# Performance work log

Measured on AMD Instinct MI355X. Metric: run time of the kernel, lower is better.

The kernel has to match this reference:

```python
import jax, jax.numpy as jnp
import numpy as np

N_NODES = 100000
N_EDGES = 1600000
G_DIM, H1, H2 = 128, 64, 32
HEADS = 4
NUM_REL = 3
NUM_CLASSES = 7


def setup_inputs() -> dict:
    key = jax.random.key(0)
    ks = jax.random.split(key, 16)
    s = 0.05
    inp = {
        "x": jax.random.normal(ks[0], (N_NODES, G_DIM), dtype=jnp.float32),
        "lengths": N_NODES,
        "edge_index": jax.random.randint(ks[1], (2, N_EDGES), 0, N_NODES),
        "edge_type": jax.random.randint(ks[2], (N_EDGES,), 0, NUM_REL),
        # RGCNConv params (root weight + per-relation weights + bias)
        "W_rel": jax.random.normal(ks[3], (NUM_REL, G_DIM, H1), dtype=jnp.float32) * s,
        "W_root": jax.random.normal(ks[4], (G_DIM, H1), dtype=jnp.float32) * s,
        "b_rgcn": jax.random.normal(ks[5], (H1,), dtype=jnp.float32) * s,
        # TransformerConv params (heads*H2 = 128 output, concat=True default)
        "Wq": jax.random.normal(ks[6], (H1, HEADS * H2), dtype=jnp.float32) * s,
        "bq": jax.random.normal(ks[7], (HEADS * H2,), dtype=jnp.float32) * s,
        "Wk": jax.random.normal(ks[8], (H1, HEADS * H2), dtype=jnp.float32) * s,
        "bk": jax.random.normal(ks[9], (HEADS * H2,), dtype=jnp.float32) * s,
        "Wv": jax.random.normal(ks[10], (H1, HEADS * H2), dtype=jnp.float32) * s,
        "bv": jax.random.normal(ks[11], (HEADS * H2,), dtype=jnp.float32) * s,
        "Wskip": jax.random.normal(ks[12], (H1, HEADS * H2), dtype=jnp.float32) * s,
        "bskip": jax.random.normal(ks[13], (HEADS * H2,), dtype=jnp.float32) * s,
        # final classifier (in = heads*H2 since TransformerConv concat=True)
        "Wf": jax.random.normal(ks[14], (HEADS * H2, NUM_CLASSES), dtype=jnp.float32) * s,
        "bf": jax.random.normal(ks[15], (NUM_CLASSES,), dtype=jnp.float32) * s,
    }
    return inp


def _forward(x, edge_index, edge_type, W_rel, W_root, b_rgcn,
             Wq, bq, Wk, bk, Wv, bv, Wskip, bskip, Wf, bf):
    n = x.shape[0]
    src, dst = edge_index[0], edge_index[1]  # source -> target flow

    # ---- RGCNConv: root transform + per-relation mean aggregation ----
    h = x @ W_root + b_rgcn  # [N, H1]
    for r in range(NUM_REL):
        hr = x @ W_rel[r]  # [N, H1] transform at node level (cheap)
        mask = (edge_type == r)
        msg = jnp.where(mask[:, None], hr[src], 0.0)  # [E, H1]
        ssum = jax.ops.segment_sum(msg, dst, num_segments=n)
        cnt = jax.ops.segment_sum(mask.astype(x.dtype), dst, num_segments=n)
        h = h + jnp.where(cnt[:, None] > 0, ssum / jnp.maximum(cnt, 1.0)[:, None], 0.0)
    h = jax.nn.relu(h)

    # ---- TransformerConv (heads=4, concat=True, root skip) ----
    Q = (h @ Wq + bq).reshape(n, HEADS, H2)
    K = (h @ Wk + bk).reshape(n, HEADS, H2)
    V = (h @ Wv + bv).reshape(n, HEADS, H2)
    scores = jnp.sum(Q[dst] * K[src], axis=-1) / jnp.sqrt(jnp.asarray(H2, x.dtype))  # [E, HEADS]
    smax = jax.ops.segment_max(scores, dst, num_segments=n)  # [N, HEADS]
    e = jnp.exp(scores - smax[dst])
    denom = jax.ops.segment_sum(e, dst, num_segments=n)  # [N, HEADS]
    alpha = e / jnp.maximum(denom[dst], 1e-16)  # [E, HEADS]
    agg = jax.ops.segment_sum(alpha[..., None] * V[src], dst, num_segments=n)  # [N, HEADS, H2]
    out = agg.reshape(n, HEADS * H2) + h @ Wskip + bskip
    out = jax.nn.relu(out)

    return out @ Wf + bf  # [N, NUM_CLASSES]


def reference(x, lengths, edge_index, edge_type, W_rel, W_root, b_rgcn,
              Wq, bq, Wk, bk, Wv, bv, Wskip, bskip, Wf, bf):
    # lengths is accepted but unused by the original forward
    return _forward(x, edge_index, edge_type, W_rel, W_root, b_rgcn,
                    Wq, bq, Wk, bk, Wv, bv, Wskip, bskip, Wf, bf)
```

## Files before the change

kernel.cpp:

```cpp
#include <hip/hip_runtime.h>
#include <math.h>

#define N_NODES 100000
#define N_EDGES 1600000

typedef short short8 __attribute__((ext_vector_type(8)));
typedef float f32x4 __attribute__((ext_vector_type(4)));

static __device__ __forceinline__ float bf2f(unsigned int u16) {
    return __uint_as_float(u16 << 16);
}
static __device__ __forceinline__ unsigned short f2bf(float f) {
    unsigned u = __float_as_uint(f);
    unsigned r = u + 0x7FFF + ((u >> 16) & 1);
    return (unsigned short)(r >> 16);
}
static __device__ __forceinline__ void unpack8(uint4 u, float* f) {
    f[0] = bf2f(u.x & 0xFFFF); f[1] = bf2f(u.x >> 16);
    f[2] = bf2f(u.y & 0xFFFF); f[3] = bf2f(u.y >> 16);
    f[4] = bf2f(u.z & 0xFFFF); f[5] = bf2f(u.z >> 16);
    f[6] = bf2f(u.w & 0xFFFF); f[7] = bf2f(u.w >> 16);
}
static __device__ __forceinline__ void unpack4(uint2 u, float* f) {
    f[0] = bf2f(u.x & 0xFFFF); f[1] = bf2f(u.x >> 16);
    f[2] = bf2f(u.y & 0xFFFF); f[3] = bf2f(u.y >> 16);
}

__global__ void repack_kernel(const float* __restrict__ Wrel, const float* __restrict__ Wroot,
                              const float* __restrict__ Wq, const float* __restrict__ Wk,
                              const float* __restrict__ Wv, const float* __restrict__ Wsk,
                              const float* __restrict__ bq, const float* __restrict__ bk,
                              const float* __restrict__ bv, const float* __restrict__ bsk,
                              unsigned short* __restrict__ W1t, unsigned short* __restrict__ W2t,
                              float* __restrict__ bcat) {
    int idx = blockIdx.x * 256 + threadIdx.x;
    if (idx < 128 * 256) {
        int k = idx >> 8, c = idx & 255;
        float v;
        if (c < 192) { int r = c >> 6, cc = c & 63; v = Wrel[r * 8192 + k * 64 + cc]; }
        else v = Wroot[k * 64 + (c - 192)];
        W1t[c * 128 + k] = f2bf(v);
    }
    int i2 = idx - 128 * 256;
    if (i2 >= 0 && i2 < 64 * 512) {
        int k = i2 >> 9, c = i2 & 511;
        float v;
        if (c < 128) v = Wq[k * 128 + c];
        else if (c < 256) v = Wk[k * 128 + c - 128];
        else if (c < 384) v = Wv[k * 128 + c - 256];
        else v = Wsk[k * 128 + c - 384];
        W2t[c * 64 + k] = f2bf(v);
    }
    int i3 = idx - 128 * 256 - 64 * 512;
    if (i3 >= 0 && i3 < 512) {
        float v;
        if (i3 < 128) v = bq[i3];
        else if (i3 < 256) v = bk[i3 - 128];
        else if (i3 < 384) v = bv[i3 - 256];
        else v = bsk[i3 - 384];
        bcat[i3] = v;
    }
}

__global__ void hist_kernel(const int* __restrict__ ei, const int* __restrict__ et,
                            int* __restrict__ cntr) {
    int e = blockIdx.x * 256 + threadIdx.x;
    if (e < N_EDGES) atomicAdd(&cntr[et[e] * N_NODES + ei[N_EDGES + e]], 1);
}

__global__ void scanA_kernel(const int* __restrict__ cntr, int* __restrict__ part) {
    __shared__ int wsum[4];
    int t = threadIdx.x;
    int base = blockIdx.x * 1024 + t * 4;
    int s = 0;
    for (int i = 0; i < 4; i++) {
        int idx = base + i;
        if (idx < N_NODES) s += cntr[idx] + cntr[N_NODES + idx] + cntr[2 * N_NODES + idx];
    }
    for (int off = 1; off < 64; off <<= 1) s += __shfl_xor(s, off);
    if ((t & 63) == 0) wsum[t >> 6] = s;
    __syncthreads();
    if (t == 0) part[blockIdx.x] = wsum[0] + wsum[1] + wsum[2] + wsum[3];
}

__global__ void scanC_kernel(const int* __restrict__ cntr, const int* __restrict__ part,
                             int* __restrict__ rs) {
    __shared__ int wsum[4];
    __shared__ int ws2[4];
    int t = threadIdx.x;
    int lane = t & 63;
    int base = blockIdx.x * 1024 + t * 4;
    int v[4]; int tsum = 0;
    for (int i = 0; i < 4; i++) {
        int idx = base + i;
        v[i] = (idx < N_NODES) ? (cntr[idx] + cntr[N_NODES + idx] + cntr[2 * N_NODES + idx]) : 0;
        tsum += v[i];
    }
    int p = (t < blockIdx.x) ? part[t] : 0;
    for (int off = 1; off < 64; off <<= 1) p += __shfl_xor(p, off);
    if (lane == 0) ws2[t >> 6] = p;
    int x = tsum;
    for (int off = 1; off < 64; off <<= 1) { int y = __shfl_up(x, off); if (lane >= off) x += y; }
    if (lane == 63) wsum[t >> 6] = x;
    __syncthreads();
    if (t == 0) { int run = 0; for (int w = 0; w < 4; w++) { int tmp = wsum[w]; wsum[w] = run; run += tmp; } }
    __syncthreads();
    int bofs = ws2[0] + ws2[1] + ws2[2] + ws2[3];
    int excl = x - tsum + wsum[t >> 6] + bofs;
    for (int i = 0; i < 4; i++) {
        int idx = base + i;
        if (idx < N_NODES) rs[idx] = excl;
        excl += v[i];
    }
    if (blockIdx.x == 0 && t == 0) rs[N_NODES] = N_EDGES;
}

__global__ void scatter_kernel(const int* __restrict__ ei, const int* __restrict__ et,
                               const int* __restrict__ rs, const int* __restrict__ cntr,
                               int* __restrict__ fill,
                               unsigned int* __restrict__ ep, float* __restrict__ epw) {
    int e = blockIdx.x * 256 + threadIdx.x;
    if (e >= N_EDGES) return;
    int src = ei[e], dst = ei[N_EDGES + e], r = et[e];
    int pos = rs[dst] + atomicAdd(&fill[dst], 1);
    int c = cntr[r * N_NODES + dst];
    ep[pos] = ((unsigned)src << 2) | (unsigned)r;
    epw[pos] = 1.f / (float)c;
}

__global__ __launch_bounds__(256) void gemm1_mfma(const float* __restrict__ X,
                                                  const unsigned short* __restrict__ W1t,
                                                  unsigned short* __restrict__ hr_all) {
    __shared__ unsigned short As[64][136];
    __shared__ unsigned short Bs[64][136];
    int t = threadIdx.x;
    int rb = blockIdx.x * 64;
    #pragma unroll
    for (int i = 0; i < 8; i++) {
        int lin = t + i * 256;
        int row = lin >> 5;
        int c4 = lin & 31;
        float4 v = make_float4(0.f, 0.f, 0.f, 0.f);
        int gr = rb + row;
        if (gr < N_NODES) v = *(const float4*)&X[gr * 128 + c4 * 4];
        unsigned w0 = (unsigned)f2bf(v.x) | ((unsigned)f2bf(v.y) << 16);
        unsigned w1 = (unsigned)f2bf(v.z) | ((unsigned)f2bf(v.w) << 16);
        *(uint2*)&As[row][c4 * 4] = make_uint2(w0, w1);
    }
    int w = t >> 6, l = t & 63;
    int wr = (w >> 1) * 32, wc = (w & 1) * 32;
    int lr = l & 15, lk = (l >> 4) * 8;
    int drow = (l >> 4) * 4;
    int dcol = l & 15;
    for (int cb4 = 0; cb4 < 4; cb4++) {
        int cb = cb4 * 64;
        __syncthreads();
        #pragma unroll
        for (int i = 0; i < 4; i++) {
            int lin = t + i * 256;
            int n = lin >> 4;
            int k8 = lin & 15;
            *(uint4*)&Bs[n][k8 * 8] = *(const uint4*)&W1t[(cb + n) * 128 + k8 * 8];
        }
        __syncthreads();
        f32x4 c00 = {0.f,0.f,0.f,0.f}, c01 = {0.f,0.f,0.f,0.f};
        f32x4 c10 = {0.f,0.f,0.f,0.f}, c11 = {0.f,0.f,0.f,0.f};
        #pragma unroll
        for (int kk = 0; kk < 128; kk += 32) {
            short8 a0 = *(const short8*)&As[wr + lr][kk + lk];
            short8 a1 = *(const short8*)&As[wr + 16 + lr][kk + lk];
            short8 b0 = *(const short8*)&Bs[wc + lr][kk + lk];
            short8 b1 = *(const short8*)&Bs[wc + 16 + lr][kk + lk];
            c00 = __builtin_amdgcn_mfma_f32_16x16x32_bf16(a0, b0, c00, 0, 0, 0);
            c01 = __builtin_amdgcn_mfma_f32_16x16x32_bf16(a0, b1, c01, 0, 0, 0);
            c10 = __builtin_amdgcn_mfma_f32_16x16x32_bf16(a1, b0, c10, 0, 0, 0);
            c11 = __builtin_amdgcn_mfma_f32_16x16x32_bf16(a1, b1, c11, 0, 0, 0);
        }
        f32x4 cc[2][2] = {{c00, c01}, {c10, c11}};
        #pragma unroll
        for (int i = 0; i < 2; i++)
            #pragma unroll
            for (int j = 0; j < 2; j++)
                #pragma unroll
                for (int rg = 0; rg < 4; rg++) {
                    int gr = rb + wr + i * 16 + drow + rg;
                    int gc = cb + wc + j * 16 + dcol;
                    if (gr < N_NODES) hr_all[gr * 256 + gc] = f2bf(cc[i][j][rg]);
                }
    }
}

__global__ __launch_bounds__(256) void rgcn_kernel(const unsigned short* __restrict__ hr,
                                                   const float* __restrict__ brg, const int* __restrict__ rs,
                                                   const unsigned int* __restrict__ ep,
                                                   const float* __restrict__ epw,
                                                   unsigned short* __restrict__ Hm) {
    int t = threadIdx.x, lane = t & 63;
    int n = blockIdx.x * 4 + (t >> 6);
    if (n >= N_NODES) return;
    int slot = lane >> 4, pos = lane & 15;
    const uint2* H2 = (const uint2*)hr;
    float a0 = 0.f, a1 = 0.f, a2 = 0.f, a3 = 0.f;
    int p0 = rs[n], p1 = rs[n + 1];
    for (int base = p0; base < p1; base += 64) {
        int pc = base + lane;
        unsigned chunk = (pc < p1) ? ep[pc] : 0u;
        float wch = (pc < p1) ? epw[pc] : 0.f;
        int cnt = min(64, p1 - base);
        for (int g0 = 0; g0 < cnt; g0 += 8) {
            int iA = g0 + slot, iB = iA + 4;
            unsigned eA = (unsigned)__shfl((int)chunk, iA);
            unsigned eB = (unsigned)__shfl((int)chunk, iB);
            float wA = __shfl(wch, iA);
            float wB = __shfl(wch, iB);
            uint2 hA = H2[eA * 16 + pos];
            uint2 hB = H2[eB * 16 + pos];
            float f[4];
            unpack4(hA, f);
            a0 += wA * f[0]; a1 += wA * f[1]; a2 += wA * f[2]; a3 += wA * f[3];
            unpack4(hB, f);
            a0 += wB * f[0]; a1 += wB * f[1]; a2 += wB * f[2]; a3 += wB * f[3];
        }
    }
    a0 += __shfl_xor(a0, 16); a0 += __shfl_xor(a0, 32);
    a1 += __shfl_xor(a1, 16); a1 += __shfl_xor(a1, 32);
    a2 += __shfl_xor(a2, 16); a2 += __shfl_xor(a2, 32);
    a3 += __shfl_xor(a3, 16); a3 += __shfl_xor(a3, 32);
    uint2 rt = H2[(n * 4 + 3) * 16 + pos];
    float rtf[4]; unpack4(rt, rtf);
    float4 bb = ((const float4*)brg)[pos];
    float h0 = fmaxf(rtf[0] + bb.x + a0, 0.f);
    float h1 = fmaxf(rtf[1] + bb.y + a1, 0.f);
    float h2 = fmaxf(rtf[2] + bb.z + a2, 0.f);
    float h3 = fmaxf(rtf[3] + bb.w + a3, 0.f);
    if (slot == 0) {
        uint2 wv;
        wv.x = (unsigned)f2bf(h0) | ((unsigned)f2bf(h1) << 16);
        wv.y = (unsigned)f2bf(h2) | ((unsigned)f2bf(h3) << 16);
        ((uint2*)Hm)[n * 16 + pos] = wv;
    }
}

__global__ __launch_bounds__(256) void gemm2_mfma(const unsigned short* __restrict__ Hm,
                                                  const unsigned short* __restrict__ W2t,
                                                  const float* __restrict__ bcat,
                                                  unsigned short* __restrict__ Qb, unsigned short* __restrict__ Kb,
                                                  unsigned short* __restrict__ Vb, unsigned short* __restrict__ Sb) {
    __shared__ unsigned short As[64][72];
    __shared__ unsigned short Bs[64][72];
    int t = threadIdx.x;
    int rb = blockIdx.x * 64;
    #pragma unroll
    for (int i = 0; i < 2; i++) {
        int lin = t + i * 256;
        int row = lin >> 3;
        int k8 = lin & 7;
        uint4 v = make_uint4(0, 0, 0, 0);
        int gr = rb + row;
        if (gr < N_NODES) v = *(const uint4*)&Hm[gr * 64 + k8 * 8];
        *(uint4*)&As[row][k8 * 8] = v;
    }
    int w = t >> 6, l = t & 63;
    int wr = (w >> 1) * 32, wc = (w & 1) * 32;
    int lr = l & 15, lk = (l >> 4) * 8;
    int drow = (l >> 4) * 4;
    int dcol = l & 15;
    for (int cb8 = 0; cb8 < 8; cb8++) {
        int cb = cb8 * 64;
        __syncthreads();
        #pragma unroll
        for (int i = 0; i < 2; i++) {
            int lin = t + i * 256;
            int n = lin >> 3;
            int k8 = lin & 7;
            *(uint4*)&Bs[n][k8 * 8] = *(const uint4*)&W2t[(cb + n) * 64 + k8 * 8];
        }
        __syncthreads();
        f32x4 c00 = {0.f,0.f,0.f,0.f}, c01 = {0.f,0.f,0.f,0.f};
        f32x4 c10 = {0.f,0.f,0.f,0.f}, c11 = {0.f,0.f,0.f,0.f};
        #pragma unroll
        for (int kk = 0; kk < 64; kk += 32) {
            short8 a0 = *(const short8*)&As[wr + lr][kk + lk];
            short8 a1 = *(const short8*)&As[wr + 16 + lr][kk + lk];
            short8 b0 = *(const short8*)&Bs[wc + lr][kk + lk];
            short8 b1 = *(const short8*)&Bs[wc + 16 + lr][kk + lk];
            c00 = __builtin_amdgcn_mfma_f32_16x16x32_bf16(a0, b0, c00, 0, 0, 0);
            c01 = __builtin_amdgcn_mfma_f32_16x16x32_bf16(a0, b1, c01, 0, 0, 0);
            c10 = __builtin_amdgcn_mfma_f32_16x16x32_bf16(a1, b0, c10, 0, 0, 0);
            c11 = __builtin_amdgcn_mfma_f32_16x16x32_bf16(a1, b1, c11, 0, 0, 0);
        }
        f32x4 cc[2][2] = {{c00, c01}, {c10, c11}};
        #pragma unroll
        for (int i = 0; i < 2; i++)
            #pragma unroll
            for (int j = 0; j < 2; j++)
                #pragma unroll
                for (int rg = 0; rg < 4; rg++) {
                    int gr = rb + wr + i * 16 + drow + rg;
                    int gc = cb + wc + j * 16 + dcol;
                    if (gr >= N_NODES) continue;
                    float v = cc[i][j][rg] + bcat[gc];
                    unsigned short h = f2bf(v);
                    if (gc < 128) Qb[gr * 128 + gc] = h;
                    else if (gc < 256) Kb[gr * 128 + (gc - 128)] = h;
                    else if (gc < 384) Vb[gr * 128 + (gc - 256)] = h;
                    else Sb[gr * 128 + (gc - 384)] = h;
                }
    }
}

__global__ __launch_bounds__(256) void attn_kernel(const unsigned short* __restrict__ Qb,
                                                   const unsigned short* __restrict__ Kb,
                                                   const unsigned short* __restrict__ Vb,
                                                   const int* __restrict__ rs, const unsigned int* __restrict__ ep,
                                                   const unsigned short* __restrict__ Sb,
                                                   const float* __restrict__ Wf, const float* __restrict__ bfv,
                                                   float* __restrict__ out) {
    int t = threadIdx.x, lane = t & 63;
    int n = blockIdx.x * 4 + (t >> 6);
    if (n >= N_NODES) return;
    int slot = lane >> 4, pos = lane & 15;
    const uint4* K4 = (const uint4*)Kb;
    const uint4* V4 = (const uint4*)Vb;
    const float qs = 0.17677669529663687f;
    uint4 qv = ((const uint4*)Qb)[n * 16 + pos];
    float q[8]; unpack8(qv, q);
    #pragma unroll
    for (int i = 0; i < 8; i++) q[i] *= qs;
    float o[8] = {0.f,0.f,0.f,0.f,0.f,0.f,0.f,0.f};
    float d = 0.f;
    int p0 = rs[n], p1 = rs[n + 1];
    for (int base = p0; base < p1; base += 64) {
        int pc = base + lane;
        unsigned chunk = (pc < p1) ? ep[pc] : 0u;
        int cnt = min(64, p1 - base);
        for (int g0 = 0; g0 < cnt; g0 += 8) {
            int iA = g0 + slot, iB = iA + 4;
            unsigned eA = (unsigned)__shfl((int)chunk, iA);
            unsigned eB = (unsigned)__shfl((int)chunk, iB);
            int sA = (int)(eA >> 2), sB = (int)(eB >> 2);
            uint4 kA = K4[sA * 16 + pos];
            uint4 vA = V4[sA * 16 + pos];
            uint4 kB = K4[sB * 16 + pos];
            uint4 vB = V4[sB * 16 + pos];
            float kf[8], vf[8];
            unpack8(kA, kf);
            float dotA = q[0]*kf[0] + q[1]*kf[1] + q[2]*kf[2] + q[3]*kf[3]
                       + q[4]*kf[4] + q[5]*kf[5] + q[6]*kf[6] + q[7]*kf[7];
            dotA += __shfl_xor(dotA, 1);
            dotA += __shfl_xor(dotA, 2);
            float wA = __expf(dotA);
            wA = (iA < cnt) ? wA : 0.f;
            unpack8(kB, kf);
            float dotB = q[0]*kf[0] + q[1]*kf[1] + q[2]*kf[2] + q[3]*kf[3]
                       + q[4]*kf[4] + q[5]*kf[5] + q[6]*kf[6] + q[7]*kf[7];
            dotB += __shfl_xor(dotB, 1);
            dotB += __shfl_xor(dotB, 2);
            float wB = __expf(dotB);
            wB = (iB < cnt) ? wB : 0.f;
            d += wA + wB;
            unpack8(vA, vf);
            #pragma unroll
            for (int i = 0; i < 8; i++) o[i] += wA * vf[i];
            unpack8(vB, vf);
            #pragma unroll
            for (int i = 0; i < 8; i++) o[i] += wB * vf[i];
        }
    }
    d += __shfl_xor(d, 16); d += __shfl_xor(d, 32);
    #pragma unroll
    for (int i = 0; i < 8; i++) { o[i] += __shfl_xor(o[i], 16); o[i] += __shfl_xor(o[i], 32); }
    float inv = (d > 0.f) ? 1.f / d : 0.f;
    uint4 sv = ((const uint4*)Sb)[n * 16 + pos];
    float sf[8]; unpack8(sv, sf);
    float rf[8];
    #pragma unroll
    for (int i = 0; i < 8; i++) rf[i] = fmaxf(sf[i] + o[i] * inv, 0.f);
    float rr0 = (slot == 0) ? rf[0] : (slot == 1) ? rf[2] : (slot == 2) ? rf[4] : rf[6];
    float rr1 = (slot == 0) ? rf[1] : (slot == 1) ? rf[3] : (slot == 2) ? rf[5] : rf[7];
    int gd = pos * 8 + slot * 2;
    float acc[7];
    #pragma unroll
    for (int j = 0; j < 7; j++) acc[j] = rr0 * Wf[gd * 7 + j] + rr1 * Wf[gd * 7 + 7 + j];
    #pragma unroll
    for (int j = 0; j < 7; j++) {
        acc[j] += __shfl_xor(acc[j], 1);
        acc[j] += __shfl_xor(acc[j], 2);
        acc[j] += __shfl_xor(acc[j], 4);
        acc[j] += __shfl_xor(acc[j], 8);
        acc[j] += __shfl_xor(acc[j], 16);
        acc[j] += __shfl_xor(acc[j], 32);
    }
    if (lane == 0) {
        #pragma unroll
        for (int j = 0; j < 7; j++) out[n * 7 + j] = acc[j] + bfv[j];
    }
}

extern "C" void kernel_launch(void* const* d_in, const int* in_sizes, int n_in,
                              void* d_out, int out_size, void* d_ws, size_t ws_size,
                              hipStream_t stream) {
    const float* x     = (const float*)d_in[0];
    const int*   ei    = (const int*)d_in[2];
    const int*   et    = (const int*)d_in[3];
    const float* Wrel  = (const float*)d_in[4];
    const float* Wroot = (const float*)d_in[5];
    const float* brg   = (const float*)d_in[6];
    const float* Wq    = (const float*)d_in[7];
    const float* bq    = (const float*)d_in[8];
    const float* Wk    = (const float*)d_in[9];
    const float* bk    = (const float*)d_in[10];
    const float* Wv    = (const float*)d_in[11];
    const float* bv    = (const float*)d_in[12];
    const float* Wsk   = (const float*)d_in[13];
    const float* bsk   = (const float*)d_in[14];
    const float* Wf    = (const float*)d_in[15];
    const float* bfv   = (const float*)d_in[16];
    float* out = (float*)d_out;

    char* ws = (char*)d_ws;
    unsigned short* hr_all = (unsigned short*)(ws + 0);
    unsigned short* Qb     = (unsigned short*)(ws + 0);
    unsigned short* Kb     = (unsigned short*)(ws + 25600000);
    unsigned short* Vb     = (unsigned short*)(ws + 51200000);
    unsigned short* Sb     = (unsigned short*)(ws + 76800000);
    unsigned short* Hm     = (unsigned short*)(ws + 102400000);
    unsigned int*   ep     = (unsigned int*)(ws + 115200000);
    float*          epw    = (float*)(ws + 121600000);
    int*            rs     = (int*)(ws + 128000000);
    int*            cntr   = (int*)(ws + 128400016);
    int*            fill   = (int*)(ws + 129600016);
    int*            part   = (int*)(ws + 130000016);
    unsigned short* W1t    = (unsigned short*)(ws + 130000528);
    unsigned short* W2t    = (unsigned short*)(ws + 130066064);
    float*          bcat   = (float*)(ws + 130131600);

    hipMemsetAsync(cntr, 0, 4 * N_NODES * sizeof(int), stream);

    repack_kernel<<<258, 256, 0, stream>>>(Wrel, Wroot, Wq, Wk, Wv, Wsk, bq, bk, bv, bsk, W1t, W2t, bcat);

    hist_kernel<<<N_EDGES / 256, 256, 0, stream>>>(ei, et, cntr);
    scanA_kernel<<<98, 256, 0, stream>>>(cntr, part);
    scanC_kernel<<<98, 256, 0, stream>>>(cntr, part, rs);
    scatter_kernel<<<N_EDGES / 256, 256, 0, stream>>>(ei, et, rs, cntr, fill, ep, epw);

    gemm1_mfma<<<1563, 256, 0, stream>>>(x, W1t, hr_all);
    rgcn_kernel<<<25000, 256, 0, stream>>>(hr_all, brg, rs, ep, epw, Hm);

    gemm2_mfma<<<1563, 256, 0, stream>>>(Hm, W2t, bcat, Qb, Kb, Vb, Sb);
    attn_kernel<<<25000, 256, 0, stream>>>(Qb, Kb, Vb, rs, ep, Sb, Wf, bfv, out);
}
```

Before: 524.3 us.

## Interleave K/V in fp16, packed-half attention math, unroll gather loops

Q/K/V/skip outputs of the second GEMM become fp16 instead of bf16. K and V are interleaved per node into one 256-wide row so the attention gather touches one contiguous region per edge, and Q and skip are paired in the same way. Q is pre-scaled by log2(e)/sqrt(d) so the softmax can use exp2 directly. The dot products and V accumulation use packed half2 arithmetic, and both gather loops are unrolled to four edges per step for more memory-level parallelism. Accumulating in fp16 and skipping the max subtraction risk precision loss or overflow.

```diff
diff --git a/kernel.cpp b/kernel.cpp
--- a/kernel.cpp
+++ b/kernel.cpp
@@ -6,6 +6,10 @@
 
 typedef short short8 __attribute__((ext_vector_type(8)));
 typedef float f32x4 __attribute__((ext_vector_type(4)));
+typedef float f32x2 __attribute__((ext_vector_type(2)));
+typedef _Float16 h2 __attribute__((ext_vector_type(2)));
+
+#define QSC 0.25503540f
 
 static __device__ __forceinline__ float bf2f(unsigned int u16) {
     return __uint_as_float(u16 << 16);
@@ -15,15 +19,25 @@
     unsigned r = u + 0x7FFF + ((u >> 16) & 1);
     return (unsigned short)(r >> 16);
 }
-static __device__ __forceinline__ void unpack8(uint4 u, float* f) {
-    f[0] = bf2f(u.x & 0xFFFF); f[1] = bf2f(u.x >> 16);
-    f[2] = bf2f(u.y & 0xFFFF); f[3] = bf2f(u.y >> 16);
-    f[4] = bf2f(u.z & 0xFFFF); f[5] = bf2f(u.z >> 16);
-    f[6] = bf2f(u.w & 0xFFFF); f[7] = bf2f(u.w >> 16);
-}
-static __device__ __forceinline__ void unpack4(uint2 u, float* f) {
-    f[0] = bf2f(u.x & 0xFFFF); f[1] = bf2f(u.x >> 16);
-    f[2] = bf2f(u.y & 0xFFFF); f[3] = bf2f(u.y >> 16);
+static __device__ __forceinline__ f32x2 bfpair(unsigned u) {
+    f32x2 r;
+    r.x = __uint_as_float(u << 16);
+    r.y = __uint_as_float(u & 0xFFFF0000u);
+    return r;
+}
+static __device__ __forceinline__ float dot8h(const h2* q, uint4 k) {
+    h2 s = q[0] * __builtin_bit_cast(h2, k.x);
+    s += q[1] * __builtin_bit_cast(h2, k.y);
+    s += q[2] * __builtin_bit_cast(h2, k.z);
+    s += q[3] * __builtin_bit_cast(h2, k.w);
+    return (float)s.x + (float)s.y;
+}
+static __device__ __forceinline__ void pv8h(h2* o, float w, uint4 v) {
+    _Float16 wh = (_Float16)w;
+    o[0] += wh * __builtin_bit_cast(h2, v.x);
+    o[1] += wh * __builtin_bit_cast(h2, v.y);
+    o[2] += wh * __builtin_bit_cast(h2, v.z);
+    o[3] += wh * __builtin_bit_cast(h2, v.w);
 }
 
 __global__ void repack_kernel(const float* __restrict__ Wrel, const float* __restrict__ Wroot,
@@ -200,43 +214,60 @@
     if (n >= N_NODES) return;
     int slot = lane >> 4, pos = lane & 15;
     const uint2* H2 = (const uint2*)hr;
-    float a0 = 0.f, a1 = 0.f, a2 = 0.f, a3 = 0.f;
+    f32x2 a01 = {0.f, 0.f}, a23 = {0.f, 0.f};
     int p0 = rs[n], p1 = rs[n + 1];
     for (int base = p0; base < p1; base += 64) {
         int pc = base + lane;
         unsigned chunk = (pc < p1) ? ep[pc] : 0u;
         float wch = (pc < p1) ? epw[pc] : 0.f;
         int cnt = min(64, p1 - base);
-        for (int g0 = 0; g0 < cnt; g0 += 8) {
+        int g0 = 0;
+        for (; g0 + 16 <= cnt; g0 += 16) {
+            int i0 = g0 + slot;
+            int e0 = __shfl((int)chunk, i0);
+            int e1 = __shfl((int)chunk, i0 + 4);
+            int e2 = __shfl((int)chunk, i0 + 8);
+            int e3 = __shfl((int)chunk, i0 + 12);
+            float w0 = __shfl(wch, i0);
+            float w1 = __shfl(wch, i0 + 4);
+            float w2 = __shfl(wch, i0 + 8);
+            float w3 = __shfl(wch, i0 + 12);
+            uint2 h0 = H2[e0 * 16 + pos];
+            uint2 h1 = H2[e1 * 16 + pos];
+            uint2 h2v = H2[e2 * 16 + pos];
+            uint2 h3 = H2[e3 * 16 + pos];
+            a01 += w0 * bfpair(h0.x); a23 += w0 * bfpair(h0.y);
+            a01 += w1 * bfpair(h1.x); a23 += w1 * bfpair(h1.y);
+            a01 += w2 * bfpair(h2v.x); a23 += w2 * bfpair(h2v.y);
+            a01 += w3 * bfpair(h3.x); a23 += w3 * bfpair(h3.y);
+        }
+        for (; g0 < cnt; g0 += 8) {
             int iA = g0 + slot, iB = iA + 4;
-            unsigned eA = (unsigned)__shfl((int)chunk, iA);
-            unsigned eB = (unsigned)__shfl((int)chunk, iB);
-            float wA = __shfl(wch, iA);
-            float wB = __shfl(wch, iB);
-            uint2 hA = H2[eA * 16 + pos];
-            uint2 hB = H2[eB * 16 + pos];
-            float f[4];
-            unpack4(hA, f);
-            a0 += wA * f[0]; a1 += wA * f[1]; a2 += wA * f[2]; a3 += wA * f[3];
-            unpack4(hB, f);
-            a0 += wB * f[0]; a1 += wB * f[1]; a2 += wB * f[2]; a3 += wB * f[3];
-        }
-    }
-    a0 += __shfl_xor(a0, 16); a0 += __shfl_xor(a0, 32);
-    a1 += __shfl_xor(a1, 16); a1 += __shfl_xor(a1, 32);
-    a2 += __shfl_xor(a2, 16); a2 += __shfl_xor(a2, 32);
-    a3 += __shfl_xor(a3, 16); a3 += __shfl_xor(a3, 32);
+            int e0 = __shfl((int)chunk, iA);
+            int e1 = __shfl((int)chunk, iB);
+            float w0 = __shfl(wch, iA);
+            float w1 = __shfl(wch, iB);
+            uint2 h0 = H2[e0 * 16 + pos];
+            uint2 h1 = H2[e1 * 16 + pos];
+            a01 += w0 * bfpair(h0.x); a23 += w0 * bfpair(h0.y);
+            a01 += w1 * bfpair(h1.x); a23 += w1 * bfpair(h1.y);
+        }
+    }
+    a01.x += __shfl_xor(a01.x, 16); a01.x += __shfl_xor(a01.x, 32);
+    a01.y += __shfl_xor(a01.y, 16); a01.y += __shfl_xor(a01.y, 32);
+    a23.x += __shfl_xor(a23.x, 16); a23.x += __shfl_xor(a23.x, 32);
+    a23.y += __shfl_xor(a23.y, 16); a23.y += __shfl_xor(a23.y, 32);
     uint2 rt = H2[(n * 4 + 3) * 16 + pos];
-    float rtf[4]; unpack4(rt, rtf);
+    f32x2 r01 = bfpair(rt.x), r23 = bfpair(rt.y);
     float4 bb = ((const float4*)brg)[pos];
-    float h0 = fmaxf(rtf[0] + bb.x + a0, 0.f);
-    float h1 = fmaxf(rtf[1] + bb.y + a1, 0.f);
-    float h2 = fmaxf(rtf[2] + bb.z + a2, 0.f);
-    float h3 = fmaxf(rtf[3] + bb.w + a3, 0.f);
+    float h0 = fmaxf(r01.x + bb.x + a01.x, 0.f);
+    float h1 = fmaxf(r01.y + bb.y + a01.y, 0.f);
+    float h2s = fmaxf(r23.x + bb.z + a23.x, 0.f);
+    float h3 = fmaxf(r23.y + bb.w + a23.y, 0.f);
     if (slot == 0) {
         uint2 wv;
         wv.x = (unsigned)f2bf(h0) | ((unsigned)f2bf(h1) << 16);
-        wv.y = (unsigned)f2bf(h2) | ((unsigned)f2bf(h3) << 16);
+        wv.y = (unsigned)f2bf(h2s) | ((unsigned)f2bf(h3) << 16);
         ((uint2*)Hm)[n * 16 + pos] = wv;
     }
 }
@@ -244,8 +275,7 @@
 __global__ __launch_bounds__(256) void gemm2_mfma(const unsigned short* __restrict__ Hm,
                                                   const unsigned short* __restrict__ W2t,
                                                   const float* __restrict__ bcat,
-                                                  unsigned short* __restrict__ Qb, unsigned short* __restrict__ Kb,
-                                                  unsigned short* __restrict__ Vb, unsigned short* __restrict__ Sb) {
+                                                  _Float16* __restrict__ QS, _Float16* __restrict__ KV) {
     __shared__ unsigned short As[64][72];
     __shared__ unsigned short Bs[64][72];
     int t = threadIdx.x;
@@ -267,6 +297,7 @@
     int dcol = l & 15;
     for (int cb8 = 0; cb8 < 8; cb8++) {
         int cb = cb8 * 64;
+        float qsc = (cb8 < 2) ? QSC : 1.f;
         __syncthreads();
         #pragma unroll
         for (int i = 0; i < 2; i++) {
@@ -299,83 +330,98 @@
                     int gr = rb + wr + i * 16 + drow + rg;
                     int gc = cb + wc + j * 16 + dcol;
                     if (gr >= N_NODES) continue;
-                    float v = cc[i][j][rg] + bcat[gc];
-                    unsigned short h = f2bf(v);
-                    if (gc < 128) Qb[gr * 128 + gc] = h;
-                    else if (gc < 256) Kb[gr * 128 + (gc - 128)] = h;
-                    else if (gc < 384) Vb[gr * 128 + (gc - 256)] = h;
-                    else Sb[gr * 128 + (gc - 384)] = h;
+                    float v = (cc[i][j][rg] + bcat[gc]) * qsc;
+                    _Float16 h = (_Float16)v;
+                    if (gc < 128) QS[gr * 256 + gc] = h;
+                    else if (gc < 384) KV[gr * 256 + gc - 128] = h;
+                    else QS[gr * 256 + gc - 256] = h;
                 }
     }
 }
 
-__global__ __launch_bounds__(256) void attn_kernel(const unsigned short* __restrict__ Qb,
-                                                   const unsigned short* __restrict__ Kb,
-                                                   const unsigned short* __restrict__ Vb,
+__global__ __launch_bounds__(256) void attn_kernel(const _Float16* __restrict__ QS,
+                                                   const _Float16* __restrict__ KV,
                                                    const int* __restrict__ rs, const unsigned int* __restrict__ ep,
-                                                   const unsigned short* __restrict__ Sb,
                                                    const float* __restrict__ Wf, const float* __restrict__ bfv,
                                                    float* __restrict__ out) {
     int t = threadIdx.x, lane = t & 63;
     int n = blockIdx.x * 4 + (t >> 6);
     if (n >= N_NODES) return;
     int slot = lane >> 4, pos = lane & 15;
-    const uint4* K4 = (const uint4*)Kb;
-    const uint4* V4 = (const uint4*)Vb;
-    const float qs = 0.17677669529663687f;
-    uint4 qv = ((const uint4*)Qb)[n * 16 + pos];
-    float q[8]; unpack8(qv, q);
-    #pragma unroll
-    for (int i = 0; i < 8; i++) q[i] *= qs;
-    float o[8] = {0.f,0.f,0.f,0.f,0.f,0.f,0.f,0.f};
+    const uint4* KV4 = (const uint4*)KV;
+    const uint4* QS4 = (const uint4*)QS;
+    uint4 qv = QS4[n * 32 + pos];
+    h2 qh[4] = { __builtin_bit_cast(h2, qv.x), __builtin_bit_cast(h2, qv.y),
+                 __builtin_bit_cast(h2, qv.z), __builtin_bit_cast(h2, qv.w) };
+    h2 o[4] = { h2{0,0}, h2{0,0}, h2{0,0}, h2{0,0} };
     float d = 0.f;
     int p0 = rs[n], p1 = rs[n + 1];
     for (int base = p0; base < p1; base += 64) {
         int pc = base + lane;
         unsigned chunk = (pc < p1) ? ep[pc] : 0u;
         int cnt = min(64, p1 - base);
-        for (int g0 = 0; g0 < cnt; g0 += 8) {
+        int g0 = 0;
+        for (; g0 + 16 <= cnt; g0 += 16) {
+            int i0 = g0 + slot;
+            int e0 = __shfl((int)chunk, i0);
+            int e1 = __shfl((int)chunk, i0 + 4);
+            int e2 = __shfl((int)chunk, i0 + 8);
+            int e3 = __shfl((int)chunk, i0 + 12);
+            int b0 = ((e0 >> 2) << 5) + pos;
+            int b1 = ((e1 >> 2) << 5) + pos;
+            int b2 = ((e2 >> 2) << 5) + pos;
+            int b3 = ((e3 >> 2) << 5) + pos;
+            uint4 k0 = KV4[b0], v0 = KV4[b0 + 16];
+            uint4 k1 = KV4[b1], v1 = KV4[b1 + 16];
+            uint4 k2 = KV4[b2], v2 = KV4[b2 + 16];
+            uint4 k3 = KV4[b3], v3 = KV4[b3 + 16];
+            float d0 = dot8h(qh, k0);
+            float d1 = dot8h(qh, k1);
+            float d2 = dot8h(qh, k2);
+            float d3 = dot8h(qh, k3);
+            d0 += __shfl_xor(d0, 1); d1 += __shfl_xor(d1, 1); d2 += __shfl_xor(d2, 1); d3 += __shfl_xor(d3, 1);
+            d0 += __shfl_xor(d0, 2); d1 += __shfl_xor(d1, 2); d2 += __shfl_xor(d2, 2); d3 += __shfl_xor(d3, 2);
+            float w0 = __builtin_amdgcn_exp2f(d0);
+            float w1 = __builtin_amdgcn_exp2f(d1);
+            float w2 = __builtin_amdgcn_exp2f(d2);
+            float w3 = __builtin_amdgcn_exp2f(d3);
+            d += (w0 + w1) + (w2 + w3);
+            pv8h(o, w0, v0); pv8h(o, w1, v1); pv8h(o, w2, v2); pv8h(o, w3, v3);
+        }
+        for (; g0 < cnt; g0 += 8) {
             int iA = g0 + slot, iB = iA + 4;
-            unsigned eA = (unsigned)__shfl((int)chunk, iA);
-            unsigned eB = (unsigned)__shfl((int)chunk, iB);
-            int sA = (int)(eA >> 2), sB = (int)(eB >> 2);
-            uint4 kA = K4[sA * 16 + pos];
-            uint4 vA = V4[sA * 16 + pos];
-            uint4 kB = K4[sB * 16 + pos];
-            uint4 vB = V4[sB * 16 + pos];
-            float kf[8], vf[8];
-            unpack8(kA, kf);
-            float dotA = q[0]*kf[0] + q[1]*kf[1] + q[2]*kf[2] + q[3]*kf[3]
-                       + q[4]*kf[4] + q[5]*kf[5] + q[6]*kf[6] + q[7]*kf[7];
-            dotA += __shfl_xor(dotA, 1);
-            dotA += __shfl_xor(dotA, 2);
-            float wA = __expf(dotA);
-            wA = (iA < cnt) ? wA : 0.f;
-            unpack8(kB, kf);
-            float dotB = q[0]*kf[0] + q[1]*kf[1] + q[2]*kf[2] + q[3]*kf[3]
-                       + q[4]*kf[4] + q[5]*kf[5] + q[6]*kf[6] + q[7]*kf[7];
-            dotB += __shfl_xor(dotB, 1);
-            dotB += __shfl_xor(dotB, 2);
-            float wB = __expf(dotB);
-            wB = (iB < cnt) ? wB : 0.f;
-            d += wA + wB;
-            unpack8(vA, vf);
-            #pragma unroll
-            for (int i = 0; i < 8; i++) o[i] += wA * vf[i];
-            unpack8(vB, vf);
-            #pragma unroll
-            for (int i = 0; i < 8; i++) o[i] += wB * vf[i];
-        }
-    }
+            int e0 = __shfl((int)chunk, iA);
+            int e1 = __shfl((int)chunk, iB);
+            int b0 = ((e0 >> 2) << 5) + pos;
+            int b1 = ((e1 >> 2) << 5) + pos;
+            uint4 k0 = KV4[b0], v0 = KV4[b0 + 16];
+            uint4 k1 = KV4[b1], v1 = KV4[b1 + 16];
+            float d0 = dot8h(qh, k0);
+            float d1 = dot8h(qh, k1);
+            d0 += __shfl_xor(d0, 1); d1 += __shfl_xor(d1, 1);
+            d0 += __shfl_xor(d0, 2); d1 += __shfl_xor(d1, 2);
+            float w0 = (iA < cnt) ? __builtin_amdgcn_exp2f(d0) : 0.f;
+            float w1 = (iB < cnt) ? __builtin_amdgcn_exp2f(d1) : 0.f;
+            d += w0 + w1;
+            pv8h(o, w0, v0); pv8h(o, w1, v1);
+        }
+    }
+    float of[8];
+    #pragma unroll
+    for (int i = 0; i < 4; i++) { of[2 * i] = (float)o[i].x; of[2 * i + 1] = (float)o[i].y; }
     d += __shfl_xor(d, 16); d += __shfl_xor(d, 32);
     #pragma unroll
-    for (int i = 0; i < 8; i++) { o[i] += __shfl_xor(o[i], 16); o[i] += __shfl_xor(o[i], 32); }
+    for (int i = 0; i < 8; i++) { of[i] += __shfl_xor(of[i], 16); of[i] += __shfl_xor(of[i], 32); }
     float inv = (d > 0.f) ? 1.f / d : 0.f;
-    uint4 sv = ((const uint4*)Sb)[n * 16 + pos];
-    float sf[8]; unpack8(sv, sf);
+    uint4 sv = QS4[n * 32 + 16 + pos];
+    h2 sh[4] = { __builtin_bit_cast(h2, sv.x), __builtin_bit_cast(h2, sv.y),
+                 __builtin_bit_cast(h2, sv.z), __builtin_bit_cast(h2, sv.w) };
     float rf[8];
     #pragma unroll
-    for (int i = 0; i < 8; i++) rf[i] = fmaxf(sf[i] + o[i] * inv, 0.f);
+    for (int i = 0; i < 4; i++) {
+        rf[2 * i]     = fmaxf((float)sh[i].x + of[2 * i] * inv, 0.f);
+        rf[2 * i + 1] = fmaxf((float)sh[i].y + of[2 * i + 1] * inv, 0.f);
+    }
     float rr0 = (slot == 0) ? rf[0] : (slot == 1) ? rf[2] : (slot == 2) ? rf[4] : rf[6];
     float rr1 = (slot == 0) ? rf[1] : (slot == 1) ? rf[3] : (slot == 2) ? rf[5] : rf[7];
     int gd = pos * 8 + slot * 2;
@@ -420,10 +466,8 @@
 
     char* ws = (char*)d_ws;
     unsigned short* hr_all = (unsigned short*)(ws + 0);
-    unsigned short* Qb     = (unsigned short*)(ws + 0);
-    unsigned short* Kb     = (unsigned short*)(ws + 25600000);
-    unsigned short* Vb     = (unsigned short*)(ws + 51200000);
-    unsigned short* Sb     = (unsigned short*)(ws + 76800000);
+    _Float16*       QS     = (_Float16*)(ws + 0);
+    _Float16*       KV     = (_Float16*)(ws + 51200000);
     unsigned short* Hm     = (unsigned short*)(ws + 102400000);
     unsigned int*   ep     = (unsigned int*)(ws + 115200000);
     float*          epw    = (float*)(ws + 121600000);
@@ -447,6 +491,6 @@
     gemm1_mfma<<<1563, 256, 0, stream>>>(x, W1t, hr_all);
     rgcn_kernel<<<25000, 256, 0, stream>>>(hr_all, brg, rs, ep, epw, Hm);
 
-    gemm2_mfma<<<1563, 256, 0, stream>>>(Hm, W2t, bcat, Qb, Kb, Vb, Sb);
-    attn_kernel<<<25000, 256, 0, stream>>>(Qb, Kb, Vb, rs, ep, Sb, Wf, bfv, out);
-}
+    gemm2_mfma<<<1563, 256, 0, stream>>>(Hm, W2t, bcat, QS, KV);
+    attn_kernel<<<25000, 256, 0, stream>>>(QS, KV, rs, ep, Wf, bfv, out);
+}
```

Measured after the change: 504.5 us. -3.8%, faster.
